# Kernel tuning notes

Measured on AMD Instinct MI355X. Metric: run time of the kernel, lower is better.

Reference implementation:

```python
import jax, jax.numpy as jnp
import numpy as np

BETA = 1.0  # inverse temperature (default of retrieve())
EPS = 1e-12  # matches torch F.normalize eps


def _l2_normalize(x):
    # torch.nn.functional.normalize(p=2, dim=-1): x / max(||x||, eps)
    n = jnp.sqrt(jnp.sum(x * x, axis=-1, keepdims=True))
    return x / jnp.maximum(n, EPS)


def setup_inputs() -> dict:
    key = jax.random.key(0)
    kq, kk = jax.random.split(key)
    N, K, D = 65536, 4096, 128
    queries = jax.random.normal(kq, (N, D), dtype=jnp.float32)
    # learnable memory keys, init_std = 0.02
    keys = jax.random.normal(kk, (K, D), dtype=jnp.float32) * 0.02
    return {"queries": queries, "keys": keys}


def reference(queries, keys):
    # normalize_keys=True, normalize_queries=True
    k_n = _l2_normalize(keys)
    q_n = _l2_normalize(queries)
    # values are TIED to the raw keys parameter (get_values returns self.keys,
    # un-normalized) — only the score-side keys are normalized.
    values = keys
    scores = BETA * jnp.einsum('nd,kd->nk', q_n, k_n)  # [N, K]
    attention = jax.nn.softmax(scores, axis=-1)
    retrieved = jnp.einsum('nk,kd->nd', attention, values)  # [N, D]
    return retrieved
```

## Files before the change

### kernel.cpp

```cpp
#include <hip/hip_runtime.h>
#include <hip/hip_bf16.h>
#include <stdint.h>


typedef __attribute__((ext_vector_type(8))) short bf16x8;
typedef __attribute__((ext_vector_type(16))) float f32x16;

#define MFMA32(a, b, c) __builtin_amdgcn_mfma_f32_32x32x16_bf16(a, b, c, 0, 0, 0)
#define ASYNC_CP16(gsrc, ldst)                                                  \
  __builtin_amdgcn_global_load_lds(                                             \
      (const __attribute__((address_space(1))) void*)(gsrc),                    \
      (__attribute__((address_space(3))) void*)(ldst), 16, 0, 0)

__device__ __forceinline__ unsigned pkbf(float lo, float hi) {
  union { __hip_bfloat162 h2; unsigned u; } v;
  v.h2 = __float22bfloat162_rn(float2{lo, hi});
  return v.u;
}

__global__ __launch_bounds__(256) void prep_k(const float* __restrict__ k,
                                              char* __restrict__ knf,
                                              char* __restrict__ vtf, int K) {
  __shared__ float sRaw[32 * 132];
  __shared__ float sScale[32];
  const int tid = threadIdx.x;
  const int kbase = blockIdx.x * 32;
  {
    const int key_loc = tid >> 3, part = tid & 7;
    const float* src = k + (size_t)(kbase + key_loc) * 128 + part * 4;
    float4 f[4];
    float ss = 0.f;
#pragma unroll
    for (int i = 0; i < 4; ++i) {
      f[i] = *(const float4*)(src + i * 32);
      ss += f[i].x * f[i].x + f[i].y * f[i].y + f[i].z * f[i].z + f[i].w * f[i].w;
    }
    ss += __shfl_xor(ss, 1);
    ss += __shfl_xor(ss, 2);
    ss += __shfl_xor(ss, 4);
    float* dst = sRaw + key_loc * 132 + part * 4;
#pragma unroll
    for (int i = 0; i < 4; ++i) *(float4*)(dst + i * 32) = f[i];
    if (part == 0) sScale[key_loc] = ss > 0.f ? rsqrtf(ss) : 0.f;
  }
  __syncthreads();

#pragma unroll
  for (int r = 0; r < 2; ++r) {
    const int c2 = r * 256 + tid;
    const int ds = c2 >> 6, l = c2 & 63;
    const int h5 = l >> 5, c32 = l & 31;
    const float sc = sScale[c32];
    const float* p = sRaw + c32 * 132 + ds * 16 + h5 * 8;
    uint4 w;
    w.x = pkbf(p[0] * sc, p[1] * sc);
    w.y = pkbf(p[2] * sc, p[3] * sc);
    w.z = pkbf(p[4] * sc, p[5] * sc);
    w.w = pkbf(p[6] * sc, p[7] * sc);
    *(uint4*)(knf + ((size_t)blockIdx.x * 512 + c2) * 16) = w;
  }
#pragma unroll
  for (int r = 0; r < 2; ++r) {
    const int c2 = r * 256 + tid;
    const int sl = c2 >> 8, db2 = (c2 >> 6) & 3, l = c2 & 63;
    const int h5 = l >> 5, c32 = l & 31;
    const int d = db2 * 32 + c32;
    const int kb = sl * 8 + h5 * 4;
    float f[8];
#pragma unroll
    for (int j = 0; j < 8; ++j)
      f[j] = sRaw[(kb + (j & 3) + (j >> 2) * 16) * 132 + d];
    uint4 w;
    w.x = pkbf(f[0], f[1]);
    w.y = pkbf(f[2], f[3]);
    w.z = pkbf(f[4], f[5]);
    w.w = pkbf(f[6], f[7]);
    *(uint4*)(vtf + ((size_t)blockIdx.x * 512 + c2) * 16) = w;
  }
}

__global__ __launch_bounds__(256, 2) void attn_main(
    const float* __restrict__ q, const char* __restrict__ knf,
    const char* __restrict__ vtf, float* __restrict__ out, int K) {
  __shared__ __align__(16) char sK[2][16384];
  __shared__ __align__(16) char sV[2][16384];
  const int tid = threadIdx.x;
  const int wave = tid >> 6, lane = tid & 63;
  const int h5 = lane >> 5, c32 = lane & 31;
  const int qrow0 = blockIdx.x * 128 + wave * 32;

  bf16x8 qf[8];
  {
    const float* qr = q + (size_t)(qrow0 + c32) * 128;
    float f[64];
    float ss = 0.f;
#pragma unroll
    for (int ds = 0; ds < 8; ++ds) {
      const float4 a = *(const float4*)(qr + ds * 16 + h5 * 8);
      const float4 b = *(const float4*)(qr + ds * 16 + h5 * 8 + 4);
      f[ds * 8 + 0] = a.x; f[ds * 8 + 1] = a.y; f[ds * 8 + 2] = a.z; f[ds * 8 + 3] = a.w;
      f[ds * 8 + 4] = b.x; f[ds * 8 + 5] = b.y; f[ds * 8 + 6] = b.z; f[ds * 8 + 7] = b.w;
    }
#pragma unroll
    for (int i = 0; i < 64; ++i) ss += f[i] * f[i];
    ss += __shfl_xor(ss, 32);
    const float sc = (ss > 0.f ? rsqrtf(ss) : 0.f) * 1.44269504f;
#pragma unroll
    for (int ds = 0; ds < 8; ++ds) {
      union { unsigned u[4]; bf16x8 v; } t;
#pragma unroll
      for (int p = 0; p < 4; ++p)
        t.u[p] = pkbf(f[ds * 8 + 2 * p] * sc, f[ds * 8 + 2 * p + 1] * sc);
      qf[ds] = t.v;
    }
  }

  f32x16 acc[4];
#pragma unroll
  for (int db2 = 0; db2 < 4; ++db2)
#pragma unroll
    for (int r = 0; r < 16; ++r) acc[db2][r] = 0.f;
  float den = 0.f;
  f32x16 Zf;
#pragma unroll
  for (int r = 0; r < 16; ++r) Zf[r] = 0.f;

  union pfu { unsigned u[4]; bf16x8 v; };
  pfu pf[4];
  f32x16 Sa[2], Sb[2];

  const int nIter = K >> 6;

  auto stageK = [&](int it, int buf) {
#pragma unroll
    for (int i = 0; i < 4; ++i)
      ASYNC_CP16(knf + (size_t)it * 16384 + (wave * 4 + i) * 1024 + lane * 16,
                 sK[buf] + (wave * 4 + i) * 1024);
  };
  auto stageV = [&](int it, int buf) {
#pragma unroll
    for (int i = 0; i < 4; ++i)
      ASYNC_CP16(vtf + (size_t)it * 16384 + (wave * 4 + i) * 1024 + lane * 16,
                 sV[buf] + (wave * 4 + i) * 1024);
  };

  auto computeS = [&](int buf, f32x16* S) {
#pragma unroll
    for (int t = 0; t < 2; ++t) {
      f32x16 s;
#pragma unroll
      for (int ds = 0; ds < 8; ++ds) {
        const bf16x8 kf = *(const bf16x8*)(sK[buf] + (t * 8 + ds) * 1024 + lane * 16);
        s = MFMA32(kf, qf[ds], (ds == 0) ? Zf : s);
      }
      S[t] = s;
    }
  };

  auto doExp = [&](const f32x16* S) {
#pragma unroll
    for (int s = 0; s < 4; ++s) {
      const int t = s >> 1, w = s & 1;
      float e[8];
#pragma unroll
      for (int j = 0; j < 8; ++j) {
        const int rr = w * 4 + (j & 3) + (j >> 2) * 8;
        e[j] = __builtin_amdgcn_exp2f(S[t][rr]);
      }
      den += ((e[0] + e[1]) + (e[2] + e[3])) + ((e[4] + e[5]) + (e[6] + e[7]));
#pragma unroll
      for (int j2 = 0; j2 < 4; ++j2) pf[s].u[j2] = pkbf(e[2 * j2], e[2 * j2 + 1]);
    }
  };

  auto doPV = [&](int buf) {
    const char* vb = sV[buf] + lane * 16;
#pragma unroll
    for (int s = 0; s < 4; ++s) {
      bf16x8 v0 = *(const bf16x8*)(vb + (s * 4 + 0) * 1024);
      bf16x8 v1 = *(const bf16x8*)(vb + (s * 4 + 1) * 1024);
      bf16x8 v2 = *(const bf16x8*)(vb + (s * 4 + 2) * 1024);
      bf16x8 v3 = *(const bf16x8*)(vb + (s * 4 + 3) * 1024);
      acc[0] = MFMA32(v0, pf[s].v, acc[0]);
      acc[1] = MFMA32(v1, pf[s].v, acc[1]);
      acc[2] = MFMA32(v2, pf[s].v, acc[2]);
      acc[3] = MFMA32(v3, pf[s].v, acc[3]);
    }
  };

  stageK(0, 0);
  stageV(0, 0);
  __syncthreads();
  stageK(1, 1);
  computeS(0, Sa);

  __syncthreads();
  stageK(2, 0);
  stageV(1, 1);
  __builtin_amdgcn_s_setprio(1);
  computeS(1, Sb);
  doExp(Sa);
  doPV(0);
  __builtin_amdgcn_s_setprio(0);

  for (int itp = 2; itp < nIter; itp += 2) {
    __syncthreads();
    stageK(itp + 1, 1);
    stageV(itp, 0);
    __builtin_amdgcn_s_setprio(1);
    computeS(0, Sa);
    doExp(Sb);
    doPV(1);
    __builtin_amdgcn_s_setprio(0);

    __syncthreads();
    if (itp + 2 < nIter) stageK(itp + 2, 0);
    stageV(itp + 1, 1);
    __builtin_amdgcn_s_setprio(1);
    computeS(1, Sb);
    doExp(Sa);
    doPV(0);
    __builtin_amdgcn_s_setprio(0);
  }

  __syncthreads();
  doExp(Sb);
  doPV(1);

  den += __shfl_xor(den, 32);
  const float rd = 1.0f / den;

  __syncthreads();
  float* wls = (float*)(&sK[0][0] + wave * 4096);
#pragma unroll
  for (int db2 = 0; db2 < 4; ++db2) {
#pragma unroll
    for (int qd = 0; qd < 4; ++qd) {
      float4 v;
      v.x = acc[db2][qd * 4 + 0] * rd;
      v.y = acc[db2][qd * 4 + 1] * rd;
      v.z = acc[db2][qd * 4 + 2] * rd;
      v.w = acc[db2][qd * 4 + 3] * rd;
      *(float4*)(wls + c32 * 32 + (((h5 + 2 * qd) ^ (c32 & 7)) << 2)) = v;
    }
#pragma unroll
    for (int p = 0; p < 4; ++p) {
      const int ql = p * 8 + (lane >> 3);
      const int x = lane & 7;
      const float4 v = *(const float4*)(wls + ql * 32 + ((x ^ (ql & 7)) << 2));
      *(float4*)(out + (size_t)(qrow0 + ql) * 128 + db2 * 32 + x * 4) = v;
    }
  }
}

extern "C" void kernel_launch(void* const* d_in, const int* in_sizes, int n_in,
                              void* d_out, int out_size, void* d_ws, size_t ws_size,
                              hipStream_t stream) {
  const float* q = (const float*)d_in[0];
  const float* k = (const float*)d_in[1];
  const int N = in_sizes[0] / 128;
  const int K = in_sizes[1] / 128;
  char* ws = (char*)d_ws;
  char* knf = ws;
  char* vtf = ws + (size_t)K * 256;
  float* out = (float*)d_out;

  prep_k<<<dim3(K / 32), dim3(256), 0, stream>>>(k, knf, vtf, K);
  attn_main<<<dim3(N / 128), dim3(256), 0, stream>>>(q, knf, vtf, out, K);
}
```

Measured before the change: 204.6 us.

## Split key dimension across two wave groups per block with cross-wave reduction

Doubles the block to 512 threads so that two groups of four waves each handle half of the keys for the same 128 query rows. The partial accumulators and denominators are then combined through shared memory at the end. The per-iteration tile shrinks to 32 keys per wave, and the pipeline is simplified to a single-S register rotation. A bit-manipulation bf16 packer replaces the intrinsic. The aim is more resident waves and lower register pressure to hide latency, at the cost of an extra reduction epilogue and a different memory layout assumption on the prepped key buffers.

```diff
diff --git a/kernel.cpp b/kernel.cpp
--- a/kernel.cpp
+++ b/kernel.cpp
@@ -16,6 +16,13 @@
   union { __hip_bfloat162 h2; unsigned u; } v;
   v.h2 = __float22bfloat162_rn(float2{lo, hi});
   return v.u;
+}
+
+__device__ __forceinline__ unsigned pkbf_fast(float lo, float hi) {
+  union { float f; unsigned u; } a{lo}, b{hi};
+  const unsigned ra = a.u + 0x7FFFu + ((a.u >> 16) & 1u);
+  const unsigned rb = b.u + 0x7FFFu + ((b.u >> 16) & 1u);
+  return (rb & 0xFFFF0000u) | (ra >> 16);
 }
 
 __global__ __launch_bounds__(256) void prep_k(const float* __restrict__ k,
@@ -79,15 +86,17 @@
   }
 }
 
-__global__ __launch_bounds__(256, 2) void attn_main(
+__global__ __launch_bounds__(512, 4) void attn_main(
     const float* __restrict__ q, const char* __restrict__ knf,
     const char* __restrict__ vtf, float* __restrict__ out, int K) {
-  __shared__ __align__(16) char sK[2][16384];
-  __shared__ __align__(16) char sV[2][16384];
+  __shared__ __align__(16) char smem[65536];
   const int tid = threadIdx.x;
   const int wave = tid >> 6, lane = tid & 63;
+  const int qsub = wave & 3, h = wave >> 2;
   const int h5 = lane >> 5, c32 = lane & 31;
-  const int qrow0 = blockIdx.x * 128 + wave * 32;
+  const int qrow0 = blockIdx.x * 128 + qsub * 32;
+  char* sKh = smem + h * 16384;
+  char* sVh = smem + 32768 + h * 16384;
 
   bf16x8 qf[8];
   {
@@ -121,134 +130,141 @@
 #pragma unroll
     for (int r = 0; r < 16; ++r) acc[db2][r] = 0.f;
   float den = 0.f;
-  f32x16 Zf;
-#pragma unroll
-  for (int r = 0; r < 16; ++r) Zf[r] = 0.f;
 
   union pfu { unsigned u[4]; bf16x8 v; };
-  pfu pf[4];
-  f32x16 Sa[2], Sb[2];
+  pfu pf[2];
 
   const int nIter = K >> 6;
+  const char* knfW = knf + ((size_t)h * nIter) * 8192 + qsub * 2048 + lane * 16;
+  const char* vtfW = vtf + ((size_t)h * nIter) * 8192 + qsub * 2048 + lane * 16;
+  char* dK = sKh + qsub * 2048;
+  char* dV = sVh + qsub * 2048;
 
   auto stageK = [&](int it, int buf) {
 #pragma unroll
-    for (int i = 0; i < 4; ++i)
-      ASYNC_CP16(knf + (size_t)it * 16384 + (wave * 4 + i) * 1024 + lane * 16,
-                 sK[buf] + (wave * 4 + i) * 1024);
+    for (int i = 0; i < 2; ++i)
+      ASYNC_CP16(knfW + (size_t)it * 8192 + i * 1024, dK + buf * 8192 + i * 1024);
   };
   auto stageV = [&](int it, int buf) {
 #pragma unroll
-    for (int i = 0; i < 4; ++i)
-      ASYNC_CP16(vtf + (size_t)it * 16384 + (wave * 4 + i) * 1024 + lane * 16,
-                 sV[buf] + (wave * 4 + i) * 1024);
-  };
-
-  auto computeS = [&](int buf, f32x16* S) {
-#pragma unroll
-    for (int t = 0; t < 2; ++t) {
-      f32x16 s;
-#pragma unroll
-      for (int ds = 0; ds < 8; ++ds) {
-        const bf16x8 kf = *(const bf16x8*)(sK[buf] + (t * 8 + ds) * 1024 + lane * 16);
-        s = MFMA32(kf, qf[ds], (ds == 0) ? Zf : s);
-      }
-      S[t] = s;
-    }
-  };
-
-  auto doExp = [&](const f32x16* S) {
-#pragma unroll
-    for (int s = 0; s < 4; ++s) {
-      const int t = s >> 1, w = s & 1;
+    for (int i = 0; i < 2; ++i)
+      ASYNC_CP16(vtfW + (size_t)it * 8192 + i * 1024, dV + buf * 8192 + i * 1024);
+  };
+
+  auto computeS = [&](int buf, f32x16& S) {
+    f32x16 s;
+#pragma unroll
+    for (int r = 0; r < 16; ++r) s[r] = 0.f;
+#pragma unroll
+    for (int ds = 0; ds < 8; ++ds) {
+      const bf16x8 kf = *(const bf16x8*)(sKh + buf * 8192 + ds * 1024 + lane * 16);
+      s = MFMA32(kf, qf[ds], s);
+    }
+    S = s;
+  };
+
+  auto doExp = [&](const f32x16& S) {
+#pragma unroll
+    for (int sl = 0; sl < 2; ++sl) {
       float e[8];
 #pragma unroll
       for (int j = 0; j < 8; ++j) {
-        const int rr = w * 4 + (j & 3) + (j >> 2) * 8;
-        e[j] = __builtin_amdgcn_exp2f(S[t][rr]);
+        const int rr = sl * 4 + (j & 3) + (j >> 2) * 8;
+        e[j] = __builtin_amdgcn_exp2f(S[rr]);
       }
       den += ((e[0] + e[1]) + (e[2] + e[3])) + ((e[4] + e[5]) + (e[6] + e[7]));
 #pragma unroll
-      for (int j2 = 0; j2 < 4; ++j2) pf[s].u[j2] = pkbf(e[2 * j2], e[2 * j2 + 1]);
+      for (int j2 = 0; j2 < 4; ++j2)
+        pf[sl].u[j2] = pkbf_fast(e[2 * j2], e[2 * j2 + 1]);
     }
   };
 
   auto doPV = [&](int buf) {
-    const char* vb = sV[buf] + lane * 16;
-#pragma unroll
-    for (int s = 0; s < 4; ++s) {
-      bf16x8 v0 = *(const bf16x8*)(vb + (s * 4 + 0) * 1024);
-      bf16x8 v1 = *(const bf16x8*)(vb + (s * 4 + 1) * 1024);
-      bf16x8 v2 = *(const bf16x8*)(vb + (s * 4 + 2) * 1024);
-      bf16x8 v3 = *(const bf16x8*)(vb + (s * 4 + 3) * 1024);
-      acc[0] = MFMA32(v0, pf[s].v, acc[0]);
-      acc[1] = MFMA32(v1, pf[s].v, acc[1]);
-      acc[2] = MFMA32(v2, pf[s].v, acc[2]);
-      acc[3] = MFMA32(v3, pf[s].v, acc[3]);
-    }
-  };
-
+    const char* vb = sVh + buf * 8192 + lane * 16;
+#pragma unroll
+    for (int sl = 0; sl < 2; ++sl) {
+      bf16x8 v0 = *(const bf16x8*)(vb + (sl * 4 + 0) * 1024);
+      bf16x8 v1 = *(const bf16x8*)(vb + (sl * 4 + 1) * 1024);
+      bf16x8 v2 = *(const bf16x8*)(vb + (sl * 4 + 2) * 1024);
+      bf16x8 v3 = *(const bf16x8*)(vb + (sl * 4 + 3) * 1024);
+      acc[0] = MFMA32(v0, pf[sl].v, acc[0]);
+      acc[1] = MFMA32(v1, pf[sl].v, acc[1]);
+      acc[2] = MFMA32(v2, pf[sl].v, acc[2]);
+      acc[3] = MFMA32(v3, pf[sl].v, acc[3]);
+    }
+  };
+
+  f32x16 S;
   stageK(0, 0);
   stageV(0, 0);
   __syncthreads();
   stageK(1, 1);
-  computeS(0, Sa);
-
-  __syncthreads();
-  stageK(2, 0);
-  stageV(1, 1);
-  __builtin_amdgcn_s_setprio(1);
-  computeS(1, Sb);
-  doExp(Sa);
-  doPV(0);
-  __builtin_amdgcn_s_setprio(0);
-
-  for (int itp = 2; itp < nIter; itp += 2) {
+  computeS(0, S);
+  doExp(S);
+
+  for (int it = 1; it < nIter; ++it) {
+    const int buf = it & 1;
     __syncthreads();
-    stageK(itp + 1, 1);
-    stageV(itp, 0);
+    if (it + 1 < nIter) stageK(it + 1, buf ^ 1);
+    stageV(it, buf);
     __builtin_amdgcn_s_setprio(1);
-    computeS(0, Sa);
-    doExp(Sb);
-    doPV(1);
+    doPV(buf ^ 1);
+    computeS(buf, S);
     __builtin_amdgcn_s_setprio(0);
-
-    __syncthreads();
-    if (itp + 2 < nIter) stageK(itp + 2, 0);
-    stageV(itp + 1, 1);
-    __builtin_amdgcn_s_setprio(1);
-    computeS(1, Sb);
-    doExp(Sa);
-    doPV(0);
-    __builtin_amdgcn_s_setprio(0);
-  }
-
-  __syncthreads();
-  doExp(Sb);
-  doPV(1);
-
-  den += __shfl_xor(den, 32);
-  const float rd = 1.0f / den;
-
-  __syncthreads();
-  float* wls = (float*)(&sK[0][0] + wave * 4096);
-#pragma unroll
-  for (int db2 = 0; db2 < 4; ++db2) {
-#pragma unroll
-    for (int qd = 0; qd < 4; ++qd) {
-      float4 v;
-      v.x = acc[db2][qd * 4 + 0] * rd;
-      v.y = acc[db2][qd * 4 + 1] * rd;
-      v.z = acc[db2][qd * 4 + 2] * rd;
-      v.w = acc[db2][qd * 4 + 3] * rd;
-      *(float4*)(wls + c32 * 32 + (((h5 + 2 * qd) ^ (c32 & 7)) << 2)) = v;
-    }
-#pragma unroll
-    for (int p = 0; p < 4; ++p) {
-      const int ql = p * 8 + (lane >> 3);
-      const int x = lane & 7;
-      const float4 v = *(const float4*)(wls + ql * 32 + ((x ^ (ql & 7)) << 2));
-      *(float4*)(out + (size_t)(qrow0 + ql) * 128 + db2 * 32 + x * 4) = v;
+    doExp(S);
+  }
+  __syncthreads();
+  doPV((nIter - 1) & 1);
+
+  float* pair = (float*)(smem + qsub * 16384);
+  __syncthreads();
+  if (h == 1) pair[lane] = den;
+  __syncthreads();
+  if (h == 0) den += pair[lane];
+  __syncthreads();
+  if (h == 1) {
+#pragma unroll
+    for (int i = 0; i < 4; ++i)
+#pragma unroll
+      for (int p2 = 0; p2 < 4; ++p2) {
+        float4 v;
+        v.x = acc[i][p2 * 4 + 0]; v.y = acc[i][p2 * 4 + 1];
+        v.z = acc[i][p2 * 4 + 2]; v.w = acc[i][p2 * 4 + 3];
+        *(float4*)((char*)pair + (i * 4 + p2) * 1024 + lane * 16) = v;
+      }
+  }
+  __syncthreads();
+  if (h == 0) {
+#pragma unroll
+    for (int i = 0; i < 4; ++i)
+#pragma unroll
+      for (int p2 = 0; p2 < 4; ++p2) {
+        const float4 v = *(const float4*)((char*)pair + (i * 4 + p2) * 1024 + lane * 16);
+        acc[i][p2 * 4 + 0] += v.x; acc[i][p2 * 4 + 1] += v.y;
+        acc[i][p2 * 4 + 2] += v.z; acc[i][p2 * 4 + 3] += v.w;
+      }
+    den += __shfl_xor(den, 32);
+    const float rd = 1.0f / den;
+
+    float* wls = pair;
+#pragma unroll
+    for (int db2 = 0; db2 < 4; ++db2) {
+#pragma unroll
+      for (int qd = 0; qd < 4; ++qd) {
+        float4 v;
+        v.x = acc[db2][qd * 4 + 0] * rd;
+        v.y = acc[db2][qd * 4 + 1] * rd;
+        v.z = acc[db2][qd * 4 + 2] * rd;
+        v.w = acc[db2][qd * 4 + 3] * rd;
+        *(float4*)(wls + c32 * 32 + (((h5 + 2 * qd) ^ (c32 & 7)) << 2)) = v;
+      }
+#pragma unroll
+      for (int p = 0; p < 4; ++p) {
+        const int ql = p * 8 + (lane >> 3);
+        const int x = lane & 7;
+        const float4 v = *(const float4*)(wls + ql * 32 + ((x ^ (ql & 7)) << 2));
+        *(float4*)(out + (size_t)(qrow0 + ql) * 128 + db2 * 32 + x * 4) = v;
+      }
     }
   }
 }
@@ -266,5 +282,5 @@
   float* out = (float*)d_out;
 
   prep_k<<<dim3(K / 32), dim3(256), 0, stream>>>(k, knf, vtf, K);
-  attn_main<<<dim3(N / 128), dim3(256), 0, stream>>>(q, knf, vtf, out, K);
-}
+  attn_main<<<dim3(N / 128), dim3(512), 0, stream>>>(q, knf, vtf, out, K);
+}
```

Result: slower. 225.4 us (+10.2%).
